# Kernel tuning notes

Measured on AMD Instinct MI355X. Metric: run time of the kernel, lower is better.

The kernel has to match this reference:

```python
import jax, jax.numpy as jnp
import numpy as np

N_NODES = 50000
N_EDGES = 800000
F_DIM = 128   # float_feat_dim
H_DIM = 64    # hidden_dim
NEG_SLOPE = 0.2


def setup_inputs() -> dict:
    key = jax.random.key(0)
    ks = jax.random.split(key, 12)
    in_dim = F_DIM + 1
    sc_in = 1.0 / np.sqrt(in_dim)
    sc_h = 1.0 / np.sqrt(H_DIM)
    return {
        "x_float": jax.random.normal(ks[0], (N_NODES, F_DIM), dtype=jnp.float32),
        "x_binary": jax.random.uniform(ks[1], (N_NODES,), dtype=jnp.float32),
        "edge_index": jax.random.randint(ks[2], (2, N_EDGES), 0, N_NODES, dtype=jnp.int64),
        "Wl": jax.random.normal(ks[3], (H_DIM, in_dim), dtype=jnp.float32) * sc_in,
        "bl": jnp.zeros((H_DIM,), dtype=jnp.float32),
        "Wr": jax.random.normal(ks[4], (H_DIM, in_dim), dtype=jnp.float32) * sc_in,
        "br": jnp.zeros((H_DIM,), dtype=jnp.float32),
        "att": jax.random.normal(ks[5], (H_DIM,), dtype=jnp.float32) * sc_h,
        "gat_bias": jnp.zeros((H_DIM,), dtype=jnp.float32),
        "Wo": jax.random.normal(ks[6], (F_DIM, H_DIM), dtype=jnp.float32) * sc_h,
        "bo": jnp.zeros((F_DIM,), dtype=jnp.float32),
        "dispersion": jnp.zeros((F_DIM,), dtype=jnp.float32),
    }


def reference(x_float, x_binary, edge_index, Wl, bl, Wr, br, att, gat_bias, Wo, bo, dispersion):
    N = x_float.shape[0]
    # concat float feats with binary feature -> [N, F+1]
    x = jnp.concatenate([x_float, x_binary[:, None]], axis=1)
    # add self loops (PyG GATv2Conv default)
    loops = jnp.arange(N, dtype=edge_index.dtype)
    src = jnp.concatenate([edge_index[0], loops])  # [E+N]
    dst = jnp.concatenate([edge_index[1], loops])
    # separate source/target linear projections (share_weights=False)
    xl = x @ Wl.T + bl  # [N, H]
    xr = x @ Wr.T + br  # [N, H]
    # per-edge GATv2 attention score: a^T LeakyReLU(x_l[j] + x_r[i])
    m = xl[src] + xr[dst]                      # [E+N, H]
    m = jnp.where(m > 0, m, NEG_SLOPE * m)
    e = m @ att                                # [E+N]
    # segment softmax over destination neighborhoods
    emax = jax.ops.segment_max(e, dst, num_segments=N)  # self loops => every seg nonempty
    ex = jnp.exp(e - emax[dst])
    denom = jax.ops.segment_sum(ex, dst, num_segments=N)
    alpha = ex / denom[dst]                    # [E+N]
    # weighted scatter-aggregate of source projections
    out = jax.ops.segment_sum(alpha[:, None] * xl[src], dst, num_segments=N) + gat_bias
    h = jax.nn.elu(out)                        # [N, H]
    logits = h @ Wo.T + bo                     # [N, F]
    return logits, jax.nn.softplus(dispersion)
```

## Files before the change

kernel.cpp:

```cpp
#include <hip/hip_runtime.h>
#include <hip/hip_bf16.h>
#include <math.h>

#define N_NODES 50000
#define N_EDGES 800000
#define F_DIM 128
#define H_DIM 64
#define IN_DIM 129
#define ETOT (N_EDGES + N_NODES)
#define NB 196
#define CAP 6144
#define EPB 3125
#define BKT_BLKS 256
#define PROJ_A 782
#define PROJ_B 781
#define AGG_BLKS 3125

typedef __hip_bfloat16 bf16;
typedef __attribute__((ext_vector_type(8))) short bf16x8;
typedef __attribute__((ext_vector_type(4))) float f32x4;

static __device__ __forceinline__ float bs2f(short s) {
    union { float f; unsigned u; } c; c.u = ((unsigned)(unsigned short)s) << 16; return c.f;
}
static __device__ __forceinline__ short f2bs(float f) {
    union { bf16 b; short s; } u; u.b = __float2bfloat16(f); return u.s;
}

static __device__ __forceinline__ void proj_body(
    int node0, short* lds,
    const float* __restrict__ xf, const float* __restrict__ xb,
    const float* __restrict__ Wl, const float* __restrict__ bl,
    const float* __restrict__ Wr, const float* __restrict__ br,
    const bf16* __restrict__ whi, const bf16* __restrict__ wlo,
    bf16* __restrict__ xl, bf16* __restrict__ xr)
{
    int wave = threadIdx.x >> 6;
    int lane = threadIdx.x & 63;
    int n = lane & 15, q = lane >> 4;

    bf16x8 bhi[2][4], blo_[2][4];
    float biasv[2], w128[2];
    #pragma unroll
    for (int nt = 0; nt < 2; ++nt) {
        int ch = wave * 32 + nt * 16 + n;
        #pragma unroll
        for (int ks = 0; ks < 4; ++ks) {
            int fid = wave * 8 + nt * 4 + ks;
            bhi[nt][ks]  = *(const bf16x8*)(whi + ((size_t)fid * 64 + lane) * 8);
            blo_[nt][ks] = *(const bf16x8*)(wlo + ((size_t)fid * 64 + lane) * 8);
        }
        biasv[nt] = (ch < 64) ? bl[ch] : br[ch - 64];
        w128[nt]  = (ch < 64) ? Wl[(size_t)ch * IN_DIM + 128]
                              : Wr[(size_t)(ch - 64) * IN_DIM + 128];
    }

    #pragma unroll
    for (int mt = 0; mt < 2; ++mt) {
        int nb = node0 + mt * 16;
        if (nb < N_NODES) {
            const float* xrow = xf + (size_t)(nb + n) * F_DIM;
            bf16x8 a[4];
            #pragma unroll
            for (int ks = 0; ks < 4; ++ks) {
                float4 u = *(const float4*)(xrow + ks * 32 + q * 8);
                float4 v = *(const float4*)(xrow + ks * 32 + q * 8 + 4);
                bf16x8 tt;
                tt[0] = f2bs(u.x); tt[1] = f2bs(u.y); tt[2] = f2bs(u.z); tt[3] = f2bs(u.w);
                tt[4] = f2bs(v.x); tt[5] = f2bs(v.y); tt[6] = f2bs(v.z); tt[7] = f2bs(v.w);
                a[ks] = tt;
            }
            f32x4 acc[2] = {{0.f,0.f,0.f,0.f},{0.f,0.f,0.f,0.f}};
            #pragma unroll
            for (int ks = 0; ks < 4; ++ks) {
                #pragma unroll
                for (int nt = 0; nt < 2; ++nt) {
                    acc[nt] = __builtin_amdgcn_mfma_f32_16x16x32_bf16(a[ks], bhi[nt][ks],  acc[nt], 0, 0, 0);
                    acc[nt] = __builtin_amdgcn_mfma_f32_16x16x32_bf16(a[ks], blo_[nt][ks], acc[nt], 0, 0, 0);
                }
            }
            float4 xbv = *(const float4*)(xb + nb + q * 4);
            float xbr[4] = {xbv.x, xbv.y, xbv.z, xbv.w};
            #pragma unroll
            for (int nt = 0; nt < 2; ++nt) {
                int ch = wave * 32 + nt * 16 + n;
                int blk = ch >> 3, pos = ch & 7;
                #pragma unroll
                for (int r = 0; r < 4; ++r) {
                    int nodeL = mt * 16 + q * 4 + r;
                    float val = acc[nt][r] + xbr[r] * w128[nt] + biasv[nt];
                    lds[nodeL * 128 + ((blk ^ (nodeL & 7)) << 3) + pos] = f2bs(val);
                }
            }
        }
    }
    __syncthreads();

    int nl = threadIdx.x >> 3, bk = threadIdx.x & 7;
    int node = node0 + nl;
    if (node < N_NODES) {
        bf16x8 v0 = *(const bf16x8*)(lds + nl * 128 + ((bk ^ (nl & 7)) << 3));
        *(bf16x8*)(xl + (size_t)node * H_DIM + bk * 8) = v0;
        bf16x8 v1 = *(const bf16x8*)(lds + nl * 128 + (((8 + bk) ^ (nl & 7)) << 3));
        *(bf16x8*)(xr + (size_t)node * H_DIM + bk * 8) = v1;
    }
}

__global__ __launch_bounds__(256) void prep_kernel(
    const float* __restrict__ Wl, const float* __restrict__ Wr,
    const float* __restrict__ Wo,
    bf16* __restrict__ whi, bf16* __restrict__ wlo,
    bf16* __restrict__ wohi, bf16* __restrict__ wolo,
    int* __restrict__ gtot)
{
    int b = blockIdx.x, t = threadIdx.x;
    if (b < 8) {
        int s = b * 256 + t;
        int fid = s >> 6, l = s & 63;
        int wave = fid >> 3, nt = (fid >> 2) & 1, ks = fid & 3;
        int ch = wave * 32 + nt * 16 + (l & 15);
        int kb = ks * 32 + (l >> 4) * 8;
        const float* wrow = (ch < 64) ? Wl + (size_t)ch * IN_DIM
                                      : Wr + (size_t)(ch - 64) * IN_DIM;
        #pragma unroll
        for (int j = 0; j < 8; ++j) {
            float v = wrow[kb + j];
            short hs = f2bs(v);
            short ls = f2bs(v - bs2f(hs));
            ((short*)whi)[(size_t)s * 8 + j] = hs;
            ((short*)wlo)[(size_t)s * 8 + j] = ls;
        }
    } else if (b < 12) {
        int s = (b - 8) * 256 + t;
        int fid = s >> 6, l = s & 63;
        int wave = fid >> 2, nt = (fid >> 1) & 1, ks = fid & 1;
        int ch = wave * 32 + nt * 16 + (l & 15);
        int kb = ks * 32 + (l >> 4) * 8;
        const float* wrow = Wo + (size_t)ch * H_DIM;
        #pragma unroll
        for (int j = 0; j < 8; ++j) {
            float v = wrow[kb + j];
            short hs = f2bs(v);
            short ls = f2bs(v - bs2f(hs));
            ((short*)wohi)[(size_t)s * 8 + j] = hs;
            ((short*)wolo)[(size_t)s * 8 + j] = ls;
        }
    } else {
        if (t < NB) gtot[t] = 0;
    }
}

__global__ __launch_bounds__(256) void h2_kernel(
    const float* __restrict__ xf, const float* __restrict__ xb,
    const float* __restrict__ Wl, const float* __restrict__ bl,
    const float* __restrict__ Wr, const float* __restrict__ br,
    const bf16* __restrict__ whi, const bf16* __restrict__ wlo,
    const int* __restrict__ esrc, const int* __restrict__ edst,
    bf16* __restrict__ xl, bf16* __restrict__ xr,
    int* __restrict__ gtot, unsigned* __restrict__ bstore2,
    int* __restrict__ bofsT)
{
    __shared__ int smem[2048];

    if (blockIdx.x < BKT_BLKS) {
        int* hist = smem;
        int* base = smem + 256;
        int* cur  = smem + 512;
        int* shs  = smem + 768;
        int t = threadIdx.x;
        int b = blockIdx.x;
        int e0 = b * EPB;
        if (t < NB) hist[t] = 0;
        __syncthreads();

        int myd[13]; int mys[13];
        #pragma unroll
        for (int i = 0; i < 13; ++i) {
            int k = t + i * 256;
            bool v = k < EPB;
            int dst = v ? edst[e0 + k] : -1;
            int sc  = v ? esrc[e0 + k] : 0;
            myd[i] = dst; mys[i] = sc;
            if (v) atomicAdd(&hist[dst >> 8], 1);
        }
        __syncthreads();

        int hv = (t < NB) ? hist[t] : 0;
        shs[t] = hv;
        __syncthreads();
        #pragma unroll
        for (int d = 1; d < 256; d <<= 1) {
            int x = (t >= d) ? shs[t - d] : 0;
            __syncthreads();
            shs[t] += x;
            __syncthreads();
        }
        if (t < NB) {
            int bs = shs[t] - hv;
            base[t] = bs;
            cur[t] = 0;
            if (hv) atomicAdd(&gtot[t], hv);
            bofsT[t * 256 + b] = (bs << 16) | hv;
        }
        __syncthreads();

        #pragma unroll
        for (int i = 0; i < 13; ++i) {
            if (myd[i] >= 0) {
                int j = myd[i] >> 8;
                int slot = base[j] + atomicAdd(&cur[j], 1);
                bstore2[(size_t)e0 + slot] =
                    ((unsigned)myd[i] << 16) | (unsigned)mys[i];
            }
        }
        return;
    }

    proj_body((blockIdx.x - BKT_BLKS) * 32, (short*)smem,
              xf, xb, Wl, bl, Wr, br, whi, wlo, xl, xr);
}

__global__ __launch_bounds__(256) void h3_kernel(
    const float* __restrict__ xf, const float* __restrict__ xb,
    const float* __restrict__ Wl, const float* __restrict__ bl,
    const float* __restrict__ Wr, const float* __restrict__ br,
    const bf16* __restrict__ whi, const bf16* __restrict__ wlo,
    bf16* __restrict__ xl, bf16* __restrict__ xr,
    const int* __restrict__ gtot, const unsigned* __restrict__ bstore2,
    const int* __restrict__ bofsT,
    int* __restrict__ offs, int* __restrict__ csr_src)
{
    __shared__ int smem3[7176];

    if (blockIdx.x < NB) {
        unsigned* ent = (unsigned*)smem3;
        int* sh    = smem3 + CAP;
        int* h256  = smem3 + CAP + 256;
        int* start = smem3 + CAP + 512;
        int* c2    = smem3 + CAP + 768;
        int* scal  = smem3 + CAP + 1024;
        int j = blockIdx.x, t = threadIdx.x;

        unsigned v = (unsigned)bofsT[j * 256 + t];
        int bbase = (int)(v >> 16);
        int bcnt  = (int)(v & 0xffffu);
        sh[t] = bcnt;
        __syncthreads();
        #pragma unroll
        for (int d = 1; d < 256; d <<= 1) {
            int x = (t >= d) ? sh[t - d] : 0;
            __syncthreads();
            sh[t] += x;
            __syncthreads();
        }
        int gb = sh[t] - bcnt;
        if (t == 255) scal[0] = sh[255];
        __syncthreads();
        int C = scal[0];

        {
            const unsigned* p = bstore2 + (size_t)t * EPB + bbase;
            for (int i = 0; i < bcnt; ++i) ent[gb + i] = p[i];
        }
        __syncthreads();

        int val = 0;
        if (t < NB) val = gtot[t] + ((t < NB - 1) ? 256 : (N_NODES - (NB - 1) * 256));
        sh[t] = val;
        __syncthreads();
        #pragma unroll
        for (int d = 1; d < 256; d <<= 1) {
            int x = (t >= d) ? sh[t - d] : 0;
            __syncthreads();
            sh[t] += x;
            __syncthreads();
        }
        if (t == j) scal[1] = sh[t] - val;
        h256[t] = 0;
        __syncthreads();
        int bb = scal[1];

        for (int k = t; k < C; k += 256)
            atomicAdd(&h256[(ent[k] >> 16) & 255], 1);
        __syncthreads();

        int node = j * 256 + t;
        int w = h256[t] + ((node < N_NODES) ? 1 : 0);
        sh[t] = w;
        __syncthreads();
        #pragma unroll
        for (int d = 1; d < 256; d <<= 1) {
            int x = (t >= d) ? sh[t - d] : 0;
            __syncthreads();
            sh[t] += x;
            __syncthreads();
        }
        int st = bb + sh[t] - w;
        start[t] = st;
        c2[t] = 0;
        if (node < N_NODES) {
            offs[node] = st;
            csr_src[st] = node;
        }
        if (j == NB - 1 && t == 0) offs[N_NODES] = ETOT;
        __syncthreads();

        for (int k = t; k < C; k += 256) {
            unsigned en = ent[k];
            int bin = (en >> 16) & 255;
            int r = atomicAdd(&c2[bin], 1);
            csr_src[start[bin] + 1 + r] = (int)(en & 0xffffu);
        }
        return;
    }

    proj_body((PROJ_A + blockIdx.x - NB) * 32, (short*)smem3,
              xf, xb, Wl, bl, Wr, br, whi, wlo, xl, xr);
}

__global__ __launch_bounds__(256) void agg_out(
    const int* __restrict__ csr_src, const int* __restrict__ offs,
    const bf16* __restrict__ xl, const bf16* __restrict__ xr,
    const float* __restrict__ att, const float* __restrict__ gb,
    const bf16* __restrict__ wohi, const bf16* __restrict__ wolo,
    const float* __restrict__ bo, const float* __restrict__ disp,
    float* __restrict__ out)
{
    __shared__ short hts[16 * 72];
    __shared__ float ldso[16 * 132];

    int wave = threadIdx.x >> 6;
    int lane = threadIdx.x & 63;
    int g  = lane >> 3;
    int c8 = lane & 7;
    int node0 = blockIdx.x * 16;

    if (blockIdx.x == 0 && threadIdx.x < F_DIM) {
        float d = disp[threadIdx.x];
        out[(size_t)N_NODES * F_DIM + threadIdx.x] = (d > 20.f) ? d : log1pf(__expf(d));
    }

    float attv[8], gbv[8];
    {
        float4 a0 = *(const float4*)(att + c8 * 8);
        float4 a1 = *(const float4*)(att + c8 * 8 + 4);
        const float L2E = 1.44269504f;
        attv[0] = a0.x * L2E; attv[1] = a0.y * L2E; attv[2] = a0.z * L2E; attv[3] = a0.w * L2E;
        attv[4] = a1.x * L2E; attv[5] = a1.y * L2E; attv[6] = a1.z * L2E; attv[7] = a1.w * L2E;
        float4 g0 = *(const float4*)(gb + c8 * 8);
        float4 g1 = *(const float4*)(gb + c8 * 8 + 4);
        gbv[0] = g0.x; gbv[1] = g0.y; gbv[2] = g0.z; gbv[3] = g0.w;
        gbv[4] = g1.x; gbv[5] = g1.y; gbv[6] = g1.z; gbv[7] = g1.w;
    }

    #pragma unroll 1
    for (int pr = 0; pr < 2; ++pr) {
        int wdA = wave * 4 + pr * 2;
        int wdB = wdA + 1;
        int widA = node0 + wdA;
        int widB = node0 + wdB;

        float xrvA[8], xrvB[8];
        {
            bf16x8 xrA = *(const bf16x8*)(xr + (size_t)widA * H_DIM + c8 * 8);
            bf16x8 xrB = *(const bf16x8*)(xr + (size_t)widB * H_DIM + c8 * 8);
            #pragma unroll
            for (int j = 0; j < 8; ++j) {
                xrvA[j] = bs2f(xrA[j]);
                xrvB[j] = bs2f(xrB[j]);
            }
        }

        int begA = offs[widA], endA = offs[widA + 1], lastA = endA - 1;
        int begB = offs[widB], endB = offs[widB + 1], lastB = endB - 1;

        float denA = 0.f, denB = 0.f;
        float accA[8] = {0.f,0.f,0.f,0.f,0.f,0.f,0.f,0.f};
        float accB[8] = {0.f,0.f,0.f,0.f,0.f,0.f,0.f,0.f};

        int iA0 = begA + g;      iA0 = (iA0 < endA) ? iA0 : lastA;
        int iA1 = begA + 8 + g;  iA1 = (iA1 < endA) ? iA1 : lastA;
        int iA2 = begA + 16 + g; iA2 = (iA2 < endA) ? iA2 : lastA;
        int iB0 = begB + g;      iB0 = (iB0 < endB) ? iB0 : lastB;
        int iB1 = begB + 8 + g;  iB1 = (iB1 < endB) ? iB1 : lastB;
        int iB2 = begB + 16 + g; iB2 = (iB2 < endB) ? iB2 : lastB;
        int sA2 = csr_src[iA2];
        int sB2 = csr_src[iB2];
        bf16x8 rA0 = *(const bf16x8*)(xl + (size_t)csr_src[iA0] * H_DIM + c8 * 8);
        bf16x8 rB0 = *(const bf16x8*)(xl + (size_t)csr_src[iB0] * H_DIM + c8 * 8);
        bf16x8 rA1 = *(const bf16x8*)(xl + (size_t)csr_src[iA1] * H_DIM + c8 * 8);
        bf16x8 rB1 = *(const bf16x8*)(xl + (size_t)csr_src[iB1] * H_DIM + c8 * 8);

        int itA = (endA - begA + 7) >> 3;
        int itB = (endB - begB + 7) >> 3;
        int nIt = (itA > itB) ? itA : itB;
        int baseA = begA, baseB = begB;

        #pragma unroll 1
        for (int it = 0; it < nIt; ++it) {
            int iA3 = baseA + 24 + g; iA3 = (iA3 < endA) ? iA3 : lastA;
            int iB3 = baseB + 24 + g; iB3 = (iB3 < endB) ? iB3 : lastB;
            int sA3 = csr_src[iA3];
            int sB3 = csr_src[iB3];
            bf16x8 rA2 = *(const bf16x8*)(xl + (size_t)sA2 * H_DIM + c8 * 8);
            bf16x8 rB2 = *(const bf16x8*)(xl + (size_t)sB2 * H_DIM + c8 * 8);

            bool vA = (baseA + g) < endA;
            bool vB = (baseB + g) < endB;
            float xvA[8], xvB[8], pA = 0.f, pB = 0.f;
            #pragma unroll
            for (int j = 0; j < 8; ++j) {
                xvA[j] = bs2f(rA0[j]);
                xvB[j] = bs2f(rB0[j]);
                float mA = xvA[j] + xrvA[j];
                float mB = xvB[j] + xrvB[j];
                mA = fmaxf(mA, 0.2f * mA);
                mB = fmaxf(mB, 0.2f * mB);
                pA += mA * attv[j];
                pB += mB * attv[j];
            }
            pA += __shfl_xor(pA, 1); pA += __shfl_xor(pA, 2); pA += __shfl_xor(pA, 4);
            pB += __shfl_xor(pB, 1); pB += __shfl_xor(pB, 2); pB += __shfl_xor(pB, 4);
            float exA = vA ? exp2f(pA) : 0.f;
            float exB = vB ? exp2f(pB) : 0.f;
            denA += exA;
            denB += exB;
            #pragma unroll
            for (int j = 0; j < 8; ++j) {
                accA[j] += exA * xvA[j];
                accB[j] += exB * xvB[j];
            }

            rA0 = rA1; rA1 = rA2; sA2 = sA3; baseA += 8;
            rB0 = rB1; rB1 = rB2; sB2 = sB3; baseB += 8;
        }

        #pragma unroll
        for (int j = 0; j < 8; ++j) {
            accA[j] += __shfl_xor(accA[j], 8);
            accA[j] += __shfl_xor(accA[j], 16);
            accA[j] += __shfl_xor(accA[j], 32);
            accB[j] += __shfl_xor(accB[j], 8);
            accB[j] += __shfl_xor(accB[j], 16);
            accB[j] += __shfl_xor(accB[j], 32);
        }
        denA += __shfl_xor(denA, 8); denA += __shfl_xor(denA, 16); denA += __shfl_xor(denA, 32);
        denB += __shfl_xor(denB, 8); denB += __shfl_xor(denB, 16); denB += __shfl_xor(denB, 32);

        if (g == 0) {
            float invA = 1.0f / denA;
            float invB = 1.0f / denB;
            bf16x8 ovA, ovB;
            #pragma unroll
            for (int j = 0; j < 8; ++j) {
                float va = accA[j] * invA + gbv[j];
                va = (va > 0.f) ? va : expm1f(va);
                ovA[j] = f2bs(va);
                float vb = accB[j] * invB + gbv[j];
                vb = (vb > 0.f) ? vb : expm1f(vb);
                ovB[j] = f2bs(vb);
            }
            *(bf16x8*)(hts + wdA * 72 + c8 * 8) = ovA;
            *(bf16x8*)(hts + wdB * 72 + c8 * 8) = ovB;
        }
    }
    __syncthreads();

    int n = lane & 15, q = lane >> 4;

    bf16x8 bhi[2][2], blo_[2][2];
    float bov[2];
    #pragma unroll
    for (int nt = 0; nt < 2; ++nt) {
        int ch = wave * 32 + nt * 16 + n;
        #pragma unroll
        for (int ks = 0; ks < 2; ++ks) {
            int fid = wave * 4 + nt * 2 + ks;
            bhi[nt][ks]  = *(const bf16x8*)(wohi + ((size_t)fid * 64 + lane) * 8);
            blo_[nt][ks] = *(const bf16x8*)(wolo + ((size_t)fid * 64 + lane) * 8);
        }
        bov[nt] = bo[ch];
    }

    bf16x8 a[2];
    #pragma unroll
    for (int ks = 0; ks < 2; ++ks)
        a[ks] = *(const bf16x8*)(hts + n * 72 + ks * 32 + q * 8);
    f32x4 acc2[2] = {{0.f,0.f,0.f,0.f},{0.f,0.f,0.f,0.f}};
    #pragma unroll
    for (int ks = 0; ks < 2; ++ks) {
        #pragma unroll
        for (int nt = 0; nt < 2; ++nt) {
            acc2[nt] = __builtin_amdgcn_mfma_f32_16x16x32_bf16(a[ks], bhi[nt][ks],  acc2[nt], 0, 0, 0);
            acc2[nt] = __builtin_amdgcn_mfma_f32_16x16x32_bf16(a[ks], blo_[nt][ks], acc2[nt], 0, 0, 0);
        }
    }
    #pragma unroll
    for (int nt = 0; nt < 2; ++nt) {
        int ch = wave * 32 + nt * 16 + n;
        #pragma unroll
        for (int r = 0; r < 4; ++r) {
            int nodeL = q * 4 + r;
            ldso[nodeL * 132 + ch] = acc2[nt][r] + bov[nt];
        }
    }
    __syncthreads();

    int nl = threadIdx.x >> 4, p = threadIdx.x & 15;
    const float* srcp = ldso + nl * 132 + p * 8;
    float* dstp = out + (size_t)(node0 + nl) * F_DIM + p * 8;
    *(float4*)(dstp)     = *(const float4*)(srcp);
    *(float4*)(dstp + 4) = *(const float4*)(srcp + 4);
}

extern "C" void kernel_launch(void* const* d_in, const int* in_sizes, int n_in,
                              void* d_out, int out_size, void* d_ws, size_t ws_size,
                              hipStream_t stream)
{
    const float* xf  = (const float*)d_in[0];
    const float* xb  = (const float*)d_in[1];
    const int*   ei  = (const int*)d_in[2];
    const float* Wl  = (const float*)d_in[3];
    const float* bl  = (const float*)d_in[4];
    const float* Wr  = (const float*)d_in[5];
    const float* br  = (const float*)d_in[6];
    const float* att = (const float*)d_in[7];
    const float* gb  = (const float*)d_in[8];
    const float* Wo  = (const float*)d_in[9];
    const float* bo  = (const float*)d_in[10];
    const float* dp  = (const float*)d_in[11];
    float* out = (float*)d_out;
    const int* esrc = ei;
    const int* edst = ei + N_EDGES;

    char* ws = (char*)d_ws;
    const size_t SZB = (size_t)N_NODES * H_DIM * sizeof(bf16);
    bf16*  xl      = (bf16*)(ws);
    bf16*  xr      = (bf16*)(ws + SZB);
    unsigned* bstore2 = (unsigned*)(ws + 2 * SZB);
    int*   csr_src = (int*)(ws + 2 * SZB + (size_t)N_EDGES * 4);
    int*   offs    = csr_src + ETOT;
    int*   gtot    = offs + (N_NODES + 4);
    int*   bofsT   = gtot + 208;
    bf16*  whi     = (bf16*)(bofsT + NB * 256);
    bf16*  wlo     = whi + 16384;
    bf16*  wohi    = wlo + 16384;
    bf16*  wolo    = wohi + 8192;

    prep_kernel<<<13, 256, 0, stream>>>(Wl, Wr, Wo, whi, wlo, wohi, wolo, gtot);

    h2_kernel<<<BKT_BLKS + PROJ_A, 256, 0, stream>>>(
        xf, xb, Wl, bl, Wr, br, whi, wlo, esrc, edst, xl, xr,
        gtot, bstore2, bofsT);

    h3_kernel<<<NB + PROJ_B, 256, 0, stream>>>(
        xf, xb, Wl, bl, Wr, br, whi, wlo, xl, xr,
        gtot, bstore2, bofsT, offs, csr_src);

    agg_out<<<AGG_BLKS, 256, 0, stream>>>(csr_src, offs, xl, xr, att, gb,
                                          wohi, wolo, bo, dp, out);
}
```

Measured before the change: 184.2 us.

## Process four destination nodes per wave with two edge lanes each

The aggregation phase used to have each wave work on two nodes at a time, spreading each node's edges across 8 lane-groups, and it ran two passes per wave. Now each wave handles four nodes at once with 16 lanes per node: 8 channel-groups times 2 edge slots. The goal is to cut the loop-bound padding caused by uneven degrees (about 17 edges on average) and to remove the outer pass loop and the long cross-lane reductions. Each node now takes more serial iterations, and the iteration count is taken as the max over the four nodes in the wave, so load imbalance and latency exposure may increase.

```diff
diff --git a/kernel.cpp b/kernel.cpp
--- a/kernel.cpp
+++ b/kernel.cpp
@@ -331,9 +331,12 @@
 
     int wave = threadIdx.x >> 6;
     int lane = threadIdx.x & 63;
-    int g  = lane >> 3;
-    int c8 = lane & 7;
+    int dl  = lane >> 4;
+    int g2  = (lane >> 3) & 1;
+    int c8  = lane & 7;
+    int wd  = wave * 4 + dl;
     int node0 = blockIdx.x * 16;
+    int wid = node0 + wd;
 
     if (blockIdx.x == 0 && threadIdx.x < F_DIM) {
         float d = disp[threadIdx.x];
@@ -353,116 +356,72 @@
         gbv[4] = g1.x; gbv[5] = g1.y; gbv[6] = g1.z; gbv[7] = g1.w;
     }
 
+    float xrv[8];
+    {
+        bf16x8 xrow = *(const bf16x8*)(xr + (size_t)wid * H_DIM + c8 * 8);
+        #pragma unroll
+        for (int j = 0; j < 8; ++j) xrv[j] = bs2f(xrow[j]);
+    }
+
+    int beg = offs[wid];
+    int end = offs[wid + 1];
+    int last = end - 1;
+
+    int nIt = (end - beg + 1) >> 1;
+    nIt = max(nIt, __shfl_xor(nIt, 16));
+    nIt = max(nIt, __shfl_xor(nIt, 32));
+
+    float den = 0.f;
+    float acc[8] = {0.f, 0.f, 0.f, 0.f, 0.f, 0.f, 0.f, 0.f};
+
+    int cur = beg + g2;
+    int i0 = cur;     i0 = (i0 < end) ? i0 : last;
+    int i1 = cur + 2; i1 = (i1 < end) ? i1 : last;
+    int i2 = cur + 4; i2 = (i2 < end) ? i2 : last;
+    int s2 = csr_src[i2];
+    bf16x8 r0 = *(const bf16x8*)(xl + (size_t)csr_src[i0] * H_DIM + c8 * 8);
+    bf16x8 r1 = *(const bf16x8*)(xl + (size_t)csr_src[i1] * H_DIM + c8 * 8);
+
     #pragma unroll 1
-    for (int pr = 0; pr < 2; ++pr) {
-        int wdA = wave * 4 + pr * 2;
-        int wdB = wdA + 1;
-        int widA = node0 + wdA;
-        int widB = node0 + wdB;
-
-        float xrvA[8], xrvB[8];
-        {
-            bf16x8 xrA = *(const bf16x8*)(xr + (size_t)widA * H_DIM + c8 * 8);
-            bf16x8 xrB = *(const bf16x8*)(xr + (size_t)widB * H_DIM + c8 * 8);
-            #pragma unroll
-            for (int j = 0; j < 8; ++j) {
-                xrvA[j] = bs2f(xrA[j]);
-                xrvB[j] = bs2f(xrB[j]);
-            }
-        }
-
-        int begA = offs[widA], endA = offs[widA + 1], lastA = endA - 1;
-        int begB = offs[widB], endB = offs[widB + 1], lastB = endB - 1;
-
-        float denA = 0.f, denB = 0.f;
-        float accA[8] = {0.f,0.f,0.f,0.f,0.f,0.f,0.f,0.f};
-        float accB[8] = {0.f,0.f,0.f,0.f,0.f,0.f,0.f,0.f};
-
-        int iA0 = begA + g;      iA0 = (iA0 < endA) ? iA0 : lastA;
-        int iA1 = begA + 8 + g;  iA1 = (iA1 < endA) ? iA1 : lastA;
-        int iA2 = begA + 16 + g; iA2 = (iA2 < endA) ? iA2 : lastA;
-        int iB0 = begB + g;      iB0 = (iB0 < endB) ? iB0 : lastB;
-        int iB1 = begB + 8 + g;  iB1 = (iB1 < endB) ? iB1 : lastB;
-        int iB2 = begB + 16 + g; iB2 = (iB2 < endB) ? iB2 : lastB;
-        int sA2 = csr_src[iA2];
-        int sB2 = csr_src[iB2];
-        bf16x8 rA0 = *(const bf16x8*)(xl + (size_t)csr_src[iA0] * H_DIM + c8 * 8);
-        bf16x8 rB0 = *(const bf16x8*)(xl + (size_t)csr_src[iB0] * H_DIM + c8 * 8);
-        bf16x8 rA1 = *(const bf16x8*)(xl + (size_t)csr_src[iA1] * H_DIM + c8 * 8);
-        bf16x8 rB1 = *(const bf16x8*)(xl + (size_t)csr_src[iB1] * H_DIM + c8 * 8);
-
-        int itA = (endA - begA + 7) >> 3;
-        int itB = (endB - begB + 7) >> 3;
-        int nIt = (itA > itB) ? itA : itB;
-        int baseA = begA, baseB = begB;
-
-        #pragma unroll 1
-        for (int it = 0; it < nIt; ++it) {
-            int iA3 = baseA + 24 + g; iA3 = (iA3 < endA) ? iA3 : lastA;
-            int iB3 = baseB + 24 + g; iB3 = (iB3 < endB) ? iB3 : lastB;
-            int sA3 = csr_src[iA3];
-            int sB3 = csr_src[iB3];
-            bf16x8 rA2 = *(const bf16x8*)(xl + (size_t)sA2 * H_DIM + c8 * 8);
-            bf16x8 rB2 = *(const bf16x8*)(xl + (size_t)sB2 * H_DIM + c8 * 8);
-
-            bool vA = (baseA + g) < endA;
-            bool vB = (baseB + g) < endB;
-            float xvA[8], xvB[8], pA = 0.f, pB = 0.f;
-            #pragma unroll
-            for (int j = 0; j < 8; ++j) {
-                xvA[j] = bs2f(rA0[j]);
-                xvB[j] = bs2f(rB0[j]);
-                float mA = xvA[j] + xrvA[j];
-                float mB = xvB[j] + xrvB[j];
-                mA = fmaxf(mA, 0.2f * mA);
-                mB = fmaxf(mB, 0.2f * mB);
-                pA += mA * attv[j];
-                pB += mB * attv[j];
-            }
-            pA += __shfl_xor(pA, 1); pA += __shfl_xor(pA, 2); pA += __shfl_xor(pA, 4);
-            pB += __shfl_xor(pB, 1); pB += __shfl_xor(pB, 2); pB += __shfl_xor(pB, 4);
-            float exA = vA ? exp2f(pA) : 0.f;
-            float exB = vB ? exp2f(pB) : 0.f;
-            denA += exA;
-            denB += exB;
-            #pragma unroll
-            for (int j = 0; j < 8; ++j) {
-                accA[j] += exA * xvA[j];
-                accB[j] += exB * xvB[j];
-            }
-
-            rA0 = rA1; rA1 = rA2; sA2 = sA3; baseA += 8;
-            rB0 = rB1; rB1 = rB2; sB2 = sB3; baseB += 8;
-        }
-
+    for (int it = 0; it < nIt; ++it) {
+        int i3 = cur + 6; i3 = (i3 < end) ? i3 : last;
+        int s3 = csr_src[i3];
+        bf16x8 r2 = *(const bf16x8*)(xl + (size_t)s2 * H_DIM + c8 * 8);
+
+        bool valid = cur < end;
+        float xv[8], p = 0.f;
         #pragma unroll
         for (int j = 0; j < 8; ++j) {
-            accA[j] += __shfl_xor(accA[j], 8);
-            accA[j] += __shfl_xor(accA[j], 16);
-            accA[j] += __shfl_xor(accA[j], 32);
-            accB[j] += __shfl_xor(accB[j], 8);
-            accB[j] += __shfl_xor(accB[j], 16);
-            accB[j] += __shfl_xor(accB[j], 32);
-        }
-        denA += __shfl_xor(denA, 8); denA += __shfl_xor(denA, 16); denA += __shfl_xor(denA, 32);
-        denB += __shfl_xor(denB, 8); denB += __shfl_xor(denB, 16); denB += __shfl_xor(denB, 32);
-
-        if (g == 0) {
-            float invA = 1.0f / denA;
-            float invB = 1.0f / denB;
-            bf16x8 ovA, ovB;
-            #pragma unroll
-            for (int j = 0; j < 8; ++j) {
-                float va = accA[j] * invA + gbv[j];
-                va = (va > 0.f) ? va : expm1f(va);
-                ovA[j] = f2bs(va);
-                float vb = accB[j] * invB + gbv[j];
-                vb = (vb > 0.f) ? vb : expm1f(vb);
-                ovB[j] = f2bs(vb);
-            }
-            *(bf16x8*)(hts + wdA * 72 + c8 * 8) = ovA;
-            *(bf16x8*)(hts + wdB * 72 + c8 * 8) = ovB;
-        }
+            xv[j] = bs2f(r0[j]);
+            float m = xv[j] + xrv[j];
+            m = fmaxf(m, 0.2f * m);
+            p += m * attv[j];
+        }
+        p += __shfl_xor(p, 1);
+        p += __shfl_xor(p, 2);
+        p += __shfl_xor(p, 4);
+        float ex = valid ? exp2f(p) : 0.f;
+        den += ex;
+        #pragma unroll
+        for (int j = 0; j < 8; ++j) acc[j] += ex * xv[j];
+
+        r0 = r1; r1 = r2; s2 = s3; cur += 2;
+    }
+
+    #pragma unroll
+    for (int j = 0; j < 8; ++j) acc[j] += __shfl_xor(acc[j], 8);
+    den += __shfl_xor(den, 8);
+
+    if (g2 == 0) {
+        float inv = 1.0f / den;
+        bf16x8 ov;
+        #pragma unroll
+        for (int j = 0; j < 8; ++j) {
+            float v = acc[j] * inv + gbv[j];
+            v = (v > 0.f) ? v : expm1f(v);
+            ov[j] = f2bs(v);
+        }
+        *(bf16x8*)(hts + wd * 72 + c8 * 8) = ov;
     }
     __syncthreads();
 
```

Measured after the change: 165.7 us. 10.0% less time.
